# Kernel optimization log

Measured on AMD Instinct MI355X. Metric: run time of the kernel, lower is better.

The kernel has to match this reference:

```python
import jax, jax.numpy as jnp
import numpy as np

B, T, I, H, O = 64, 512, 512, 512, 512

def setup_inputs() -> dict:
    key = jax.random.key(0)
    ks = jax.random.split(key, 8)
    s = lambda k, shape, fan: jax.random.normal(k, shape, dtype=jnp.float32) / np.sqrt(fan)
    return {
        "embeddings": jax.random.normal(ks[0], (B, T, I), dtype=jnp.float32),
        "last_logits": jax.random.normal(ks[1], (B, O), dtype=jnp.float32),
        "W_in": s(ks[2], (H, I), I),
        "b_in": jnp.zeros((H,), jnp.float32),
        "W_y": s(ks[3], (H, O), O),
        "b_y": jnp.zeros((H,), jnp.float32),
        "W_out": s(ks[4], (O, H), H),
        "b_out": jnp.zeros((O,), jnp.float32),
    }

def reference(embeddings, last_logits, W_in, b_in, W_y, b_y, W_out, b_out):
    # Precompute input projection for all timesteps: [B,T,H] -> scan axis [T,B,H]
    xin = jnp.einsum("bti,hi->bth", embeddings, W_in) + b_in
    xin = jnp.swapaxes(xin, 0, 1)  # [T,B,H]

    def step(y_t, xin_t):
        # Jordan cell: h_t = tanh(W_in x_t + W_y y_{t-1} + biases); y_t = W_out h_t + b_out
        h_t = jnp.tanh(xin_t + y_t @ W_y.T + b_y)
        y_new = h_t @ W_out.T + b_out
        return y_new, (h_t, y_new)

    y_last, (h_seq, y_seq) = jax.lax.scan(step, last_logits, xin)
    h = jnp.swapaxes(h_seq, 0, 1)  # [B,T,H]
    y = jnp.swapaxes(y_seq, 0, 1)  # [B,T,O]
    return h, y, y_last
```

## Files before the change

### kernel.cpp

```cpp
#include <hip/hip_runtime.h>
#include <hip/hip_bf16.h>
#include <stdint.h>

typedef unsigned short u16;
typedef unsigned int u32;
typedef unsigned long long u64;
typedef __attribute__((ext_vector_type(8))) short short8;
typedef __attribute__((ext_vector_type(4))) float f32x4;
typedef __attribute__((ext_vector_type(4))) unsigned short u16x4;

__device__ __forceinline__ float bf2f(u16 h) {
    union { u32 u; float f; } c; c.u = ((u32)h) << 16; return c.f;
}
__device__ __forceinline__ u16 f2bf(float f) {
    union { float f; u32 u; } c; c.f = f;
    u32 u = c.u;
    return (u16)((u + 0x7fffu + ((u >> 16) & 1u)) >> 16);
}

__global__ void k_init(int* flags) { flags[threadIdx.x] = 0; }

__global__ void k_c(const float* __restrict__ Wy, const float* __restrict__ bout,
                    const float* __restrict__ bin, const float* __restrict__ by,
                    float* __restrict__ cvec, float* __restrict__ biasE) {
    int i = blockIdx.x * 64 + threadIdx.x;
    const float* wr = Wy + (size_t)i * 512;
    float s = 0.f;
    for (int k = 0; k < 512; ++k) s += wr[k] * bout[k];
    cvec[i] = s;
    biasE[i] = s + bin[i] + by[i];
}

__global__ __launch_bounds__(512) void k_z0(const float* __restrict__ ll,
                                            const float* __restrict__ Wy,
                                            const float* __restrict__ cvec,
                                            float* __restrict__ z0mc) {
    __shared__ float lls[512];
    int b = blockIdx.x, i = threadIdx.x;
    lls[i] = ll[b * 512 + i];
    __syncthreads();
    const float* wr = Wy + (size_t)i * 512;
    float s = 0.f;
    for (int k = 0; k < 512; ++k) s += wr[k] * lls[k];
    z0mc[(size_t)b * 512 + i] = s - cvec[i];
}

__global__ __launch_bounds__(256) void k_split(const float* __restrict__ in,
                                               u16* __restrict__ hi,
                                               u16* __restrict__ lo) {
    int i = blockIdx.x * 256 + threadIdx.x;
    float v = in[i];
    u16 h = f2bf(v);
    hi[i] = h;
    lo[i] = f2bf(v - bf2f(h));
}

__global__ __launch_bounds__(256) void k_tsplit(const float* __restrict__ in,
                                                u16* __restrict__ hi,
                                                u16* __restrict__ lo) {
    __shared__ float tile[32][33];
    int bx = blockIdx.x, by = blockIdx.y;
    int tx = threadIdx.x & 31, ty = threadIdx.x >> 5;
    for (int i = 0; i < 32; i += 8)
        tile[ty + i][tx] = in[(size_t)(by * 32 + ty + i) * 512 + bx * 32 + tx];
    __syncthreads();
    for (int i = 0; i < 32; i += 8) {
        float v = tile[tx][ty + i];
        size_t idx = (size_t)(bx * 32 + ty + i) * 512 + by * 32 + tx;
        u16 h = f2bf(v);
        hi[idx] = h;
        lo[idx] = f2bf(v - bf2f(h));
    }
}

__global__ __launch_bounds__(256) void gemm3(
    const void* __restrict__ Aptr, int a_fp32,
    const u16* __restrict__ Bhi, const u16* __restrict__ Blo,
    u16* __restrict__ out_hi, u16* __restrict__ out_lo,
    float* __restrict__ out_f,
    const float* __restrict__ bias, int mode) {
    __shared__ u16 AsHi[128 * 32];
    __shared__ u16 AsLo[128 * 32];
    __shared__ u16 BsHi[128 * 32];
    __shared__ u16 BsLo[128 * 32];
    const int tid = threadIdx.x;
    const int lane = tid & 63;
    const int w = tid >> 6;
    const int wm = w & 1, wn = w >> 1;
    const int quad = lane >> 4, l15 = lane & 15;
    const int tx = blockIdx.x, tn = blockIdx.y;

    f32x4 acc[4][4];
    f32x4 zero4 = {0.f, 0.f, 0.f, 0.f};
#pragma unroll
    for (int i = 0; i < 4; ++i)
#pragma unroll
        for (int j = 0; j < 4; ++j) acc[i][j] = zero4;

    const float* Af = (const float*)Aptr;
    const u16* Ab = (const u16*)Aptr;
    const int s0 = tid, s1 = tid + 256;

    for (int kk = 0; kk < 16; ++kk) {
        const uint4* BgH = (const uint4*)(Bhi + (size_t)tn * 128 * 512 + kk * 32);
        const uint4* BgL = (const uint4*)(Blo + (size_t)tn * 128 * 512 + kk * 32);
        uint4 bh0 = BgH[(s0 >> 2) * 64 + (s0 & 3)];
        uint4 bh1 = BgH[(s1 >> 2) * 64 + (s1 & 3)];
        uint4 bl0 = BgL[(s0 >> 2) * 64 + (s0 & 3)];
        uint4 bl1 = BgL[(s1 >> 2) * 64 + (s1 & 3)];
        f32x4 av[4];
        uint4 ab0, ab1;
        if (a_fp32) {
            const float* Agf = Af + (size_t)tx * 128 * 512 + kk * 32;
#pragma unroll
            for (int p = 0; p < 4; ++p) {
                int f = tid + p * 256;
                av[p] = *(const f32x4*)(Agf + (f >> 3) * 512 + (f & 7) * 4);
            }
        } else {
            const uint4* Ag = (const uint4*)(Ab + (size_t)tx * 128 * 512 + kk * 32);
            ab0 = Ag[(s0 >> 2) * 64 + (s0 & 3)];
            ab1 = Ag[(s1 >> 2) * 64 + (s1 & 3)];
        }
        __syncthreads();
        ((uint4*)BsHi)[s0] = bh0; ((uint4*)BsHi)[s1] = bh1;
        ((uint4*)BsLo)[s0] = bl0; ((uint4*)BsLo)[s1] = bl1;
        if (a_fp32) {
#pragma unroll
            for (int p = 0; p < 4; ++p) {
                int f = tid + p * 256;
                u16x4 hi4, lo4;
#pragma unroll
                for (int j = 0; j < 4; ++j) {
                    float v = av[p][j];
                    u16 hh = f2bf(v);
                    hi4[j] = hh;
                    lo4[j] = f2bf(v - bf2f(hh));
                }
                int off = (f >> 3) * 32 + (f & 7) * 4;
                *(u16x4*)(AsHi + off) = hi4;
                *(u16x4*)(AsLo + off) = lo4;
            }
        } else {
            ((uint4*)AsHi)[s0] = ab0;
            ((uint4*)AsHi)[s1] = ab1;
        }
        __syncthreads();

        short8 afh[4], afl[4], bfh[4], bfl[4];
#pragma unroll
        for (int mi = 0; mi < 4; ++mi) {
            afh[mi] = *(const short8*)(AsHi + (wm * 64 + mi * 16 + l15) * 32 + quad * 8);
            if (a_fp32)
                afl[mi] = *(const short8*)(AsLo + (wm * 64 + mi * 16 + l15) * 32 + quad * 8);
        }
#pragma unroll
        for (int ni = 0; ni < 4; ++ni) {
            bfh[ni] = *(const short8*)(BsHi + (wn * 64 + ni * 16 + l15) * 32 + quad * 8);
            bfl[ni] = *(const short8*)(BsLo + (wn * 64 + ni * 16 + l15) * 32 + quad * 8);
        }
#pragma unroll
        for (int mi = 0; mi < 4; ++mi)
#pragma unroll
            for (int ni = 0; ni < 4; ++ni) {
                acc[mi][ni] = __builtin_amdgcn_mfma_f32_16x16x32_bf16(
                    afh[mi], bfh[ni], acc[mi][ni], 0, 0, 0);
                acc[mi][ni] = __builtin_amdgcn_mfma_f32_16x16x32_bf16(
                    afh[mi], bfl[ni], acc[mi][ni], 0, 0, 0);
                if (a_fp32)
                    acc[mi][ni] = __builtin_amdgcn_mfma_f32_16x16x32_bf16(
                        afl[mi], bfh[ni], acc[mi][ni], 0, 0, 0);
            }
    }

#pragma unroll
    for (int mi = 0; mi < 4; ++mi) {
#pragma unroll
        for (int ni = 0; ni < 4; ++ni) {
            int col = tn * 128 + wn * 64 + ni * 16 + l15;
            float bv = (mode == 1) ? bias[col] : 0.f;
#pragma unroll
            for (int r = 0; r < 4; ++r) {
                int row = tx * 128 + wm * 64 + mi * 16 + quad * 4 + r;
                float v = acc[mi][ni][r] + bv;
                size_t idx = (size_t)row * 512 + col;
                if (mode == 0) {
                    u16 hi = f2bf(v);
                    out_hi[idx] = hi;
                    out_lo[idx] = f2bf(v - bf2f(hi));
                } else {
                    out_f[idx] = v;
                }
            }
        }
    }
}

__global__ __launch_bounds__(256, 1) void k_scan(
    const u16* __restrict__ Mhi, const u16* __restrict__ Mlo,
    float* e_io,
    const float* __restrict__ z0mc,
    u32* h_ex,
    int* flags)
{
    __shared__ float zpart[2 * 4 * 4 * 64];

    const int tid = threadIdx.x;
    const int lane = tid & 63, w = tid >> 6;
    const int quad = lane >> 4, l15 = lane & 15;
    const int g = blockIdx.x & 3, s = blockIdx.x >> 2;

    short8 mf[2][4][2];
#pragma unroll
    for (int nt = 0; nt < 2; ++nt)
#pragma unroll
        for (int kap = 0; kap < 4; ++kap) {
            size_t off = ((size_t)(s * 32 + nt * 16 + l15)) * 512 +
                         (w * 128 + kap * 32 + quad * 8);
            mf[nt][kap][0] = *(const short8*)(Mhi + off);
            mf[nt][kap][1] = *(const short8*)(Mlo + off);
        }

    const int erow = tid >> 4;
    const int ec0 = (tid & 15) * 2;
    const int bb = g * 16 + erow;

#pragma unroll 1
    for (int t = 0; t < 512; ++t) {
        if (t > 0) {
            const u64* ex = (const u64*)(h_ex +
                (size_t)(((t - 1) & 1) * 4 + g) * 8192);
            f32x4 acc[2];
            f32x4 zero4 = {0.f, 0.f, 0.f, 0.f};
            acc[0] = zero4; acc[1] = zero4;
#pragma unroll
            for (int kap = 0; kap < 4; ++kap) {
                const u64* p = ex + (l15 * 512 + w * 128 + kap * 32 + quad * 8) / 2;
                u64 d0 = __hip_atomic_load(p + 0, __ATOMIC_RELAXED,
                                           __HIP_MEMORY_SCOPE_AGENT);
                u64 d1 = __hip_atomic_load(p + 1, __ATOMIC_RELAXED,
                                           __HIP_MEMORY_SCOPE_AGENT);
                u64 d2 = __hip_atomic_load(p + 2, __ATOMIC_RELAXED,
                                           __HIP_MEMORY_SCOPE_AGENT);
                u64 d3 = __hip_atomic_load(p + 3, __ATOMIC_RELAXED,
                                           __HIP_MEMORY_SCOPE_AGENT);
                u32 qs[8] = {(u32)d0, (u32)(d0 >> 32), (u32)d1, (u32)(d1 >> 32),
                             (u32)d2, (u32)(d2 >> 32), (u32)d3, (u32)(d3 >> 32)};
                short8 ahi, alo;
#pragma unroll
                for (int j = 0; j < 8; ++j) {
                    ahi[j] = (short)(qs[j] & 0xffffu);
                    alo[j] = (short)(qs[j] >> 16);
                }
#pragma unroll
                for (int nt = 0; nt < 2; ++nt) {
                    acc[nt] = __builtin_amdgcn_mfma_f32_16x16x32_bf16(
                        ahi, mf[nt][kap][0], acc[nt], 0, 0, 0);
                    acc[nt] = __builtin_amdgcn_mfma_f32_16x16x32_bf16(
                        alo, mf[nt][kap][0], acc[nt], 0, 0, 0);
                    acc[nt] = __builtin_amdgcn_mfma_f32_16x16x32_bf16(
                        ahi, mf[nt][kap][1], acc[nt], 0, 0, 0);
                }
            }
#pragma unroll
            for (int nt = 0; nt < 2; ++nt)
#pragma unroll
                for (int r = 0; r < 4; ++r)
                    zpart[((nt * 4 + w) * 4 + r) * 64 + lane] = acc[nt][r];
        }
        __syncthreads();

        {
            float hv[2];
#pragma unroll
            for (int cc = 0; cc < 2; ++cc) {
                int col = ec0 + cc;
                int gcol = s * 32 + col;
                size_t idx = ((size_t)bb * 512 + t) * 512 + gcol;
                float ev = e_io[idx];
                float z;
                if (t == 0) {
                    z = z0mc[(size_t)bb * 512 + gcol];
                } else {
                    int nt = col >> 4;
                    int lp = (erow >> 2) * 16 + (col & 15);
                    int rg = erow & 3;
                    z = zpart[((nt * 4 + 0) * 4 + rg) * 64 + lp] +
                        zpart[((nt * 4 + 1) * 4 + rg) * 64 + lp] +
                        zpart[((nt * 4 + 2) * 4 + rg) * 64 + lp] +
                        zpart[((nt * 4 + 3) * 4 + rg) * 64 + lp];
                }
                float hval = tanhf(z + ev);
                e_io[idx] = hval;
                hv[cc] = hval;
            }
            u32 pk[2];
#pragma unroll
            for (int cc = 0; cc < 2; ++cc) {
                u16 hi = f2bf(hv[cc]);
                u16 lo = f2bf(hv[cc] - bf2f(hi));
                pk[cc] = (((u32)lo) << 16) | (u32)hi;
            }
            u64 val = ((u64)pk[1] << 32) | pk[0];
            u64* dst = (u64*)(h_ex + (size_t)((t & 1) * 4 + g) * 8192 +
                              erow * 512 + s * 32 + ec0);
            __hip_atomic_store(dst, val, __ATOMIC_RELAXED,
                               __HIP_MEMORY_SCOPE_AGENT);
        }
        __syncthreads();
        __asm__ volatile("" ::: "memory");
        if (tid == 0)
            __hip_atomic_store(&flags[g * 16 + s], t + 1, __ATOMIC_RELAXED,
                               __HIP_MEMORY_SCOPE_AGENT);
        if (w == 0 && lane < 16) {
            while (__hip_atomic_load(&flags[g * 16 + lane], __ATOMIC_RELAXED,
                                     __HIP_MEMORY_SCOPE_AGENT) < t + 1)
                __builtin_amdgcn_s_sleep(1);
        }
        __syncthreads();
        __asm__ volatile("" ::: "memory");
    }
}

__global__ __launch_bounds__(512) void k_ylast(const float* __restrict__ yreg,
                                               float* __restrict__ ylast) {
    int b = blockIdx.x, o = threadIdx.x;
    ylast[(size_t)b * 512 + o] = yreg[((size_t)b * 512 + 511) * 512 + o];
}

extern "C" void kernel_launch(void* const* d_in, const int* in_sizes, int n_in,
                              void* d_out, int out_size, void* d_ws, size_t ws_size,
                              hipStream_t stream) {
    const float* emb  = (const float*)d_in[0];
    const float* ll   = (const float*)d_in[1];
    const float* Win  = (const float*)d_in[2];
    const float* bin  = (const float*)d_in[3];
    const float* Wy   = (const float*)d_in[4];
    const float* by   = (const float*)d_in[5];
    const float* Wout = (const float*)d_in[6];
    const float* bout = (const float*)d_in[7];

    float* out = (float*)d_out;
    float* h_reg = out;
    float* y_reg = out + (size_t)16777216;
    float* ylast_reg = out + (size_t)33554432;

    char* ws = (char*)d_ws;
    size_t off = 0;
    u16* buf1 = (u16*)(ws + off); off += (size_t)512 * 512 * 2;
    u16* buf2 = (u16*)(ws + off); off += (size_t)512 * 512 * 2;
    u16* Mhi  = (u16*)(ws + off); off += (size_t)512 * 512 * 2;
    u16* Mlo  = (u16*)(ws + off); off += (size_t)512 * 512 * 2;
    float* z0mc  = (float*)(ws + off); off += (size_t)64 * 512 * 4;
    float* cvec  = (float*)(ws + off); off += 512 * 4;
    float* biasE = (float*)(ws + off); off += 512 * 4;
    u32* h_ex = (u32*)(ws + off); off += (size_t)2 * 4 * 8192 * 4;
    int* flags = (int*)(ws + off); off += 64 * 4;

    k_init<<<1, 64, 0, stream>>>(flags);
    k_c<<<8, 64, 0, stream>>>(Wy, bout, bin, by, cvec, biasE);
    k_z0<<<64, 512, 0, stream>>>(ll, Wy, cvec, z0mc);
    k_tsplit<<<dim3(16, 16), 256, 0, stream>>>(Wout, buf1, buf2);
    gemm3<<<dim3(4, 4), 256, 0, stream>>>(Wy, 1, buf1, buf2, Mhi, Mlo,
                                          nullptr, nullptr, 0);
    k_split<<<1024, 256, 0, stream>>>(Win, buf1, buf2);
    gemm3<<<dim3(256, 4), 256, 0, stream>>>(emb, 1, buf1, buf2, nullptr, nullptr,
                                            h_reg, biasE, 1);
    k_scan<<<64, 256, 0, stream>>>(Mhi, Mlo, h_reg, z0mc, h_ex, flags);
    k_split<<<1024, 256, 0, stream>>>(Wout, buf1, buf2);
    gemm3<<<dim3(256, 4), 256, 0, stream>>>(h_reg, 1, buf1, buf2, nullptr, nullptr,
                                            y_reg, bout, 1);
    k_ylast<<<64, 512, 0, stream>>>(y_reg, ylast_reg);
}
```

Baseline: 2.260 ms.

## Replace flag-based grid barrier in scan with tag bits embedded in exchanged data

```diff
diff --git a/kernel.cpp b/kernel.cpp
--- a/kernel.cpp
+++ b/kernel.cpp
@@ -7,6 +7,7 @@
 typedef unsigned long long u64;
 typedef __attribute__((ext_vector_type(8))) short short8;
 typedef __attribute__((ext_vector_type(4))) float f32x4;
+typedef __attribute__((ext_vector_type(2))) float f32x2;
 typedef __attribute__((ext_vector_type(4))) unsigned short u16x4;
 
 __device__ __forceinline__ float bf2f(u16 h) {
@@ -18,7 +19,23 @@
     return (u16)((u + 0x7fffu + ((u >> 16) & 1u)) >> 16);
 }
 
-__global__ void k_init(int* flags) { flags[threadIdx.x] = 0; }
+__device__ __forceinline__ float fast_tanh(float x) {
+    float ax = __builtin_fabsf(x);
+    float arg = ax * 2.8853900817779268f;
+    float p;
+    asm("v_exp_f32 %0, %1" : "=v"(p) : "v"(arg));
+    float q = p + 1.f;
+    float r;
+    asm("v_rcp_f32 %0, %1" : "=v"(r) : "v"(q));
+    float t = 1.f - 2.f * r;
+    return __builtin_copysignf(t, x);
+}
+
+__global__ void k_init(u32* h_ex) {
+    uint4 v;
+    v.x = 0x00010000u; v.y = 0x00010000u; v.z = 0x00010000u; v.w = 0x00010000u;
+    ((uint4*)h_ex)[blockIdx.x * 256 + threadIdx.x] = v;
+}
 
 __global__ void k_c(const float* __restrict__ Wy, const float* __restrict__ bout,
                     const float* __restrict__ bin, const float* __restrict__ by,
@@ -200,8 +217,7 @@
     const u16* __restrict__ Mhi, const u16* __restrict__ Mlo,
     float* e_io,
     const float* __restrict__ z0mc,
-    u32* h_ex,
-    int* flags)
+    u32* h_ex)
 {
     __shared__ float zpart[2 * 4 * 4 * 64];
 
@@ -225,27 +241,43 @@
     const int ec0 = (tid & 15) * 2;
     const int bb = g * 16 + erow;
 
+    f32x2 ecur = *(const f32x2*)(e_io + ((size_t)bb * 512 + 0) * 512 + s * 32 + ec0);
+
 #pragma unroll 1
     for (int t = 0; t < 512; ++t) {
         if (t > 0) {
             const u64* ex = (const u64*)(h_ex +
                 (size_t)(((t - 1) & 1) * 4 + g) * 8192);
+            const u64* p0 = ex + (size_t)(l15 * 512 + w * 128 + quad * 8) / 2;
+            const u64 tagmask = (1ull << 16) | (1ull << 48);
+            const u64 tagval = (((t - 1) >> 1) & 1) ? tagmask : 0ull;
+            u64 d[4][4];
+            for (;;) {
+#pragma unroll
+                for (int kap = 0; kap < 4; ++kap) {
+                    const u64* p = p0 + kap * 16;
+#pragma unroll
+                    for (int j = 0; j < 4; ++j)
+                        d[kap][j] = __hip_atomic_load(p + j, __ATOMIC_RELAXED,
+                                                      __HIP_MEMORY_SCOPE_AGENT);
+                }
+                u64 bad = 0;
+#pragma unroll
+                for (int kap = 0; kap < 4; ++kap)
+#pragma unroll
+                    for (int j = 0; j < 4; ++j)
+                        bad |= (d[kap][j] ^ tagval) & tagmask;
+                if (__all(bad == 0)) break;
+            }
             f32x4 acc[2];
             f32x4 zero4 = {0.f, 0.f, 0.f, 0.f};
             acc[0] = zero4; acc[1] = zero4;
 #pragma unroll
             for (int kap = 0; kap < 4; ++kap) {
-                const u64* p = ex + (l15 * 512 + w * 128 + kap * 32 + quad * 8) / 2;
-                u64 d0 = __hip_atomic_load(p + 0, __ATOMIC_RELAXED,
-                                           __HIP_MEMORY_SCOPE_AGENT);
-                u64 d1 = __hip_atomic_load(p + 1, __ATOMIC_RELAXED,
-                                           __HIP_MEMORY_SCOPE_AGENT);
-                u64 d2 = __hip_atomic_load(p + 2, __ATOMIC_RELAXED,
-                                           __HIP_MEMORY_SCOPE_AGENT);
-                u64 d3 = __hip_atomic_load(p + 3, __ATOMIC_RELAXED,
-                                           __HIP_MEMORY_SCOPE_AGENT);
-                u32 qs[8] = {(u32)d0, (u32)(d0 >> 32), (u32)d1, (u32)(d1 >> 32),
-                             (u32)d2, (u32)(d2 >> 32), (u32)d3, (u32)(d3 >> 32)};
+                u32 qs[8] = {(u32)d[kap][0], (u32)(d[kap][0] >> 32),
+                             (u32)d[kap][1], (u32)(d[kap][1] >> 32),
+                             (u32)d[kap][2], (u32)(d[kap][2] >> 32),
+                             (u32)d[kap][3], (u32)(d[kap][3] >> 32)};
                 short8 ahi, alo;
 #pragma unroll
                 for (int j = 0; j < 8; ++j) {
@@ -275,12 +307,9 @@
 #pragma unroll
             for (int cc = 0; cc < 2; ++cc) {
                 int col = ec0 + cc;
-                int gcol = s * 32 + col;
-                size_t idx = ((size_t)bb * 512 + t) * 512 + gcol;
-                float ev = e_io[idx];
                 float z;
                 if (t == 0) {
-                    z = z0mc[(size_t)bb * 512 + gcol];
+                    z = z0mc[(size_t)bb * 512 + s * 32 + col];
                 } else {
                     int nt = col >> 4;
                     int lp = (erow >> 2) * 16 + (col & 15);
@@ -290,15 +319,15 @@
                         zpart[((nt * 4 + 2) * 4 + rg) * 64 + lp] +
                         zpart[((nt * 4 + 3) * 4 + rg) * 64 + lp];
                 }
-                float hval = tanhf(z + ev);
-                e_io[idx] = hval;
-                hv[cc] = hval;
-            }
+                hv[cc] = fast_tanh(z + ecur[cc]);
+            }
+            u32 tag = (u32)((t >> 1) & 1);
             u32 pk[2];
 #pragma unroll
             for (int cc = 0; cc < 2; ++cc) {
                 u16 hi = f2bf(hv[cc]);
                 u16 lo = f2bf(hv[cc] - bf2f(hi));
+                lo = (u16)((lo & 0xFFFEu) | tag);
                 pk[cc] = (((u32)lo) << 16) | (u32)hi;
             }
             u64 val = ((u64)pk[1] << 32) | pk[0];
@@ -306,18 +335,14 @@
                               erow * 512 + s * 32 + ec0);
             __hip_atomic_store(dst, val, __ATOMIC_RELAXED,
                                __HIP_MEMORY_SCOPE_AGENT);
-        }
-        __syncthreads();
+            size_t idx = ((size_t)bb * 512 + t) * 512 + s * 32 + ec0;
+            f32x2 hw; hw[0] = hv[0]; hw[1] = hv[1];
+            *(f32x2*)(e_io + idx) = hw;
+            if (t < 511)
+                ecur = *(const f32x2*)(e_io + idx + 512);
+        }
         __asm__ volatile("" ::: "memory");
-        if (tid == 0)
-            __hip_atomic_store(&flags[g * 16 + s], t + 1, __ATOMIC_RELAXED,
-                               __HIP_MEMORY_SCOPE_AGENT);
-        if (w == 0 && lane < 16) {
-            while (__hip_atomic_load(&flags[g * 16 + lane], __ATOMIC_RELAXED,
-                                     __HIP_MEMORY_SCOPE_AGENT) < t + 1)
-                __builtin_amdgcn_s_sleep(1);
-        }
-        __syncthreads();
+        __builtin_amdgcn_s_barrier();
         __asm__ volatile("" ::: "memory");
     }
 }
@@ -355,9 +380,8 @@
     float* cvec  = (float*)(ws + off); off += 512 * 4;
     float* biasE = (float*)(ws + off); off += 512 * 4;
     u32* h_ex = (u32*)(ws + off); off += (size_t)2 * 4 * 8192 * 4;
-    int* flags = (int*)(ws + off); off += 64 * 4;
-
-    k_init<<<1, 64, 0, stream>>>(flags);
+
+    k_init<<<64, 256, 0, stream>>>(h_ex);
     k_c<<<8, 64, 0, stream>>>(Wy, bout, bin, by, cvec, biasE);
     k_z0<<<64, 512, 0, stream>>>(ll, Wy, cvec, z0mc);
     k_tsplit<<<dim3(16, 16), 256, 0, stream>>>(Wout, buf1, buf2);
@@ -366,7 +390,7 @@
     k_split<<<1024, 256, 0, stream>>>(Win, buf1, buf2);
     gemm3<<<dim3(256, 4), 256, 0, stream>>>(emb, 1, buf1, buf2, nullptr, nullptr,
                                             h_reg, biasE, 1);
-    k_scan<<<64, 256, 0, stream>>>(Mhi, Mlo, h_reg, z0mc, h_ex, flags);
+    k_scan<<<64, 256, 0, stream>>>(Mhi, Mlo, h_reg, z0mc, h_ex);
     k_split<<<1024, 256, 0, stream>>>(Wout, buf1, buf2);
     gemm3<<<dim3(256, 4), 256, 0, stream>>>(h_reg, 1, buf1, buf2, nullptr, nullptr,
                                             y_reg, bout, 1);
```

Result: no change. 2.240 ms (-0.9%).
